# Kernel optimization log

Measured on AMD Instinct MI355X. Metric: run time of the kernel, lower is better.

The kernel has to match this reference:

```python
import jax, jax.numpy as jnp
import numpy as np

N_ATOMS = 50000
N_EDGES = 320000
ATOM_DIM = 32
BOND_DIM = 64


def setup_inputs() -> dict:
    key = jax.random.key(0)
    k1, k2, k3, k4 = jax.random.split(key, 4)
    atom_features = jax.random.normal(k1, (N_ATOMS, ATOM_DIM), dtype=jnp.float32)
    bond_features = jax.random.normal(k2, (N_EDGES, BOND_DIM), dtype=jnp.float32)
    pair_indices = jax.random.randint(k3, (N_EDGES, 2), 0, N_ATOMS, dtype=jnp.int64)
    # Xavier-uniform init for kernel [bond_dim, atom_dim*atom_dim]
    fan_in, fan_out = BOND_DIM, ATOM_DIM * ATOM_DIM
    limit = float(np.sqrt(6.0 / (fan_in + fan_out)))
    kernel = jax.random.uniform(k4, (BOND_DIM, ATOM_DIM * ATOM_DIM), dtype=jnp.float32,
                                minval=-limit, maxval=limit)
    bias = jnp.zeros((ATOM_DIM * ATOM_DIM,), dtype=jnp.float32)
    return {"atom_features": atom_features, "bond_features": bond_features,
            "pair_indices": pair_indices, "kernel": kernel, "bias": bias}


def reference(atom_features, bond_features, pair_indices, kernel, bias):
    d = atom_features.shape[-1]
    # Dense projection: [E, bond_dim] @ [bond_dim, d*d] -> [E, d, d]
    edge_mat = (bond_features @ kernel + bias).reshape(-1, d, d)
    # Gather neighbor features and apply per-edge matrix-vector product
    nbr = atom_features[pair_indices[:, 1]]              # [E, d]
    transformed = jnp.einsum('eij,ej->ei', edge_mat, nbr)  # [E, d]
    # Scatter-add aggregation onto destination atoms
    return jax.ops.segment_sum(transformed, pair_indices[:, 0],
                               num_segments=atom_features.shape[0])
```

## Files before the change

kernel.cpp:

```cpp
#include <hip/hip_runtime.h>
#include <stdint.h>

#define NA 50000
#define NE 320000
#define AD 32
#define BD 64

#define WS_FLAG   0
#define WS_COUNTS 16
#define WS_CURSOR (WS_COUNTS + NA)
#define WS_OFFS   (WS_CURSOR + NA)
#define WS_EIDS   150048

__device__ __forceinline__ void load_pair(const void* p, int e, int mode, int& s, int& d){
  if (mode){ const int* q = (const int*)p; s = q[2*e]; d = q[2*e+1]; }
  else     { const long long* q = (const long long*)p; s = (int)q[2*e]; d = (int)q[2*e+1]; }
}

__global__ void k_detect(const void* pairs, uint32_t* ws){
  const uint32_t* w = (const uint32_t*)pairs;
  uint32_t x = 0;
  for (int i = threadIdx.x; i < 2048; i += 256) x |= w[2*i + 1];
  __shared__ uint32_t sh[256];
  sh[threadIdx.x] = x; __syncthreads();
  for (int s = 128; s > 0; s >>= 1){
    if (threadIdx.x < s) sh[threadIdx.x] |= sh[threadIdx.x + s];
    __syncthreads();
  }
  if (threadIdx.x == 0) ws[WS_FLAG] = (sh[0] != 0u) ? 1u : 0u;
}

__global__ void k_hist(const void* pairs, uint32_t* ws){
  int e = blockIdx.x * 256 + threadIdx.x;
  if (e >= NE) return;
  int mode = (int)ws[WS_FLAG];
  int s, d; load_pair(pairs, e, mode, s, d);
  atomicAdd(&ws[WS_COUNTS + s], 1u);
}

__global__ void k_scan(uint32_t* ws){
  const uint32_t* counts = ws + WS_COUNTS;
  uint32_t* offs = ws + WS_OFFS;
  __shared__ uint32_t wsum[16];
  __shared__ uint32_t carrysh;
  const int tid = threadIdx.x; const int lane = tid & 63; const int wid = tid >> 6;
  if (tid == 0) carrysh = 0u;
  __syncthreads();
  for (int base = 0; base < NA; base += 8192){
    uint32_t v[8]; uint32_t tot = 0u;
    int i0 = base + tid * 8;
    #pragma unroll
    for (int j = 0; j < 8; ++j){ int i = i0 + j; v[j] = (i < NA) ? counts[i] : 0u; tot += v[j]; }
    uint32_t inc = tot;
    #pragma unroll
    for (int m = 1; m < 64; m <<= 1){ uint32_t t = __shfl_up(inc, m); if (lane >= m) inc += t; }
    if (lane == 63) wsum[wid] = inc;
    __syncthreads();
    if (wid == 0){
      uint32_t w = (lane < 16) ? wsum[lane] : 0u;
      #pragma unroll
      for (int m = 1; m < 16; m <<= 1){ uint32_t t = __shfl_up(w, m); if (lane >= m) w += t; }
      if (lane < 16) wsum[lane] = w;
    }
    __syncthreads();
    uint32_t waveoff = (wid == 0) ? 0u : wsum[wid - 1];
    uint32_t run = carrysh + waveoff + (inc - tot);
    #pragma unroll
    for (int j = 0; j < 8; ++j){ int i = i0 + j; if (i < NA) offs[i] = run; run += v[j]; }
    __syncthreads();
    if (tid == 0) carrysh += wsum[15];
    __syncthreads();
  }
  if (tid == 0) offs[NA] = carrysh;
}

__global__ void k_scatter(const void* pairs, uint32_t* ws){
  int e = blockIdx.x * 256 + threadIdx.x;
  if (e >= NE) return;
  int mode = (int)ws[WS_FLAG];
  int s, d; load_pair(pairs, e, mode, s, d);
  uint32_t p = atomicAdd(&ws[WS_CURSOR + s], 1u);
  ws[WS_EIDS + ws[WS_OFFS + s] + p] = (uint32_t)e;
}

__launch_bounds__(512)
__global__ void k_main(const float* __restrict__ atoms, const float* __restrict__ bonds,
                       const void* __restrict__ pairs, const float* __restrict__ Kg,
                       const float* __restrict__ bias, float* __restrict__ out,
                       const uint32_t* __restrict__ ws){
  __shared__ float Ksh[8 * 1024];
  __shared__ float red[8 * 520];

  const int tid  = threadIdx.x;
  const int lane = tid & 63;
  const int wid  = tid >> 6;
  const int kk   = lane & 7;
  const int jq   = lane >> 3;
  const int mode = (int)ws[WS_FLAG];
  const uint32_t* offs = ws + WS_OFFS;
  const uint32_t* eids = ws + WS_EIDS;

  const int a0 = blockIdx.x * 16 + wid * 2;
  const int a1 = a0 + 1;

  float R0[8][4], R1[8][4], S0[4], S1[4];
  #pragma unroll
  for (int c = 0; c < 8; ++c)
    #pragma unroll
    for (int j = 0; j < 4; ++j){ R0[c][j] = 0.f; R1[c][j] = 0.f; }
  #pragma unroll
  for (int j = 0; j < 4; ++j){ S0[j] = 0.f; S1[j] = 0.f; }

  #pragma unroll
  for (int sel = 0; sel < 2; ++sel){
    const int a = sel ? a1 : a0;
    const uint32_t beg = offs[a], end = offs[a + 1];
    for (uint32_t t = beg; t < end; ++t){
      const int e = (int)eids[t];
      int s_, d_; load_pair(pairs, e, mode, s_, d_);
      const float4 av = *(const float4*)&atoms[d_ * AD + jq * 4];
      float b[8];
      #pragma unroll
      for (int c = 0; c < 8; ++c) b[c] = bonds[e * BD + c * 8 + kk];
      if (sel == 0){
        #pragma unroll
        for (int c = 0; c < 8; ++c){
          R0[c][0] += b[c] * av.x; R0[c][1] += b[c] * av.y;
          R0[c][2] += b[c] * av.z; R0[c][3] += b[c] * av.w;
        }
        if (kk == 0){ S0[0] += av.x; S0[1] += av.y; S0[2] += av.z; S0[3] += av.w; }
      } else {
        #pragma unroll
        for (int c = 0; c < 8; ++c){
          R1[c][0] += b[c] * av.x; R1[c][1] += b[c] * av.y;
          R1[c][2] += b[c] * av.z; R1[c][3] += b[c] * av.w;
        }
        if (kk == 0){ S1[0] += av.x; S1[1] += av.y; S1[2] += av.z; S1[3] += av.w; }
      }
    }
  }

  float acc0[32], acc1[32];
  #pragma unroll
  for (int i = 0; i < 32; ++i){ acc0[i] = 0.f; acc1[i] = 0.f; }

  #pragma unroll
  for (int c = 0; c < 8; ++c){
    __syncthreads();
    #pragma unroll
    for (int q = 0; q < 4; ++q){
      int f4 = tid + q * 512;
      int word = f4 * 4;
      int row = word >> 10;
      int col = word & 1023;
      *(float4*)&Ksh[word] = *(const float4*)&Kg[(8 * c + row) * 1024 + col];
    }
    __syncthreads();
    #pragma unroll
    for (int i = 0; i < 32; ++i){
      const float4 kv = *(const float4*)&Ksh[kk * 1024 + i * 32 + jq * 4];
      acc0[i] += kv.x * R0[c][0] + kv.y * R0[c][1] + kv.z * R0[c][2] + kv.w * R0[c][3];
      acc1[i] += kv.x * R1[c][0] + kv.y * R1[c][1] + kv.z * R1[c][2] + kv.w * R1[c][3];
    }
  }

  if (kk == 0){
    #pragma unroll
    for (int i = 0; i < 32; ++i){
      const float4 bv = *(const float4*)&bias[i * 32 + jq * 4];
      acc0[i] += bv.x * S0[0] + bv.y * S0[1] + bv.z * S0[2] + bv.w * S0[3];
      acc1[i] += bv.x * S1[0] + bv.y * S1[1] + bv.z * S1[2] + bv.w * S1[3];
    }
  }

  float* myred = &red[wid * 520];
  auto epi = [&](const float (&acc)[32], int a){
    #pragma unroll
    for (int g = 0; g < 4; ++g){
      #pragma unroll
      for (int ii = 0; ii < 8; ++ii) myred[ii * 65 + lane] = acc[g * 8 + ii];
      const int ii = lane & 7, seg = lane >> 3;
      float p = 0.f;
      #pragma unroll
      for (int t2 = 0; t2 < 8; ++t2) p += myred[ii * 65 + seg * 8 + t2];
      p += __shfl_xor(p, 8);
      p += __shfl_xor(p, 16);
      p += __shfl_xor(p, 32);
      if (lane < 8) out[a * 32 + g * 8 + lane] = p;
    }
  };
  epi(acc0, a0);
  epi(acc1, a1);
}

extern "C" void kernel_launch(void* const* d_in, const int* in_sizes, int n_in,
                              void* d_out, int out_size, void* d_ws, size_t ws_size,
                              hipStream_t stream){
  const float* atoms = (const float*)d_in[0];
  const float* bonds = (const float*)d_in[1];
  const void*  pairs = d_in[2];
  const float* Kg    = (const float*)d_in[3];
  const float* bias  = (const float*)d_in[4];
  float* out = (float*)d_out;
  uint32_t* ws = (uint32_t*)d_ws;

  hipMemsetAsync(ws + WS_COUNTS, 0, sizeof(uint32_t) * 2 * NA, stream);
  k_detect<<<1, 256, 0, stream>>>(pairs, ws);
  k_hist<<<(NE + 255) / 256, 256, 0, stream>>>(pairs, ws);
  k_scan<<<1, 1024, 0, stream>>>(ws);
  k_scatter<<<(NE + 255) / 256, 256, 0, stream>>>(pairs, ws);
  k_main<<<NA / 16, 512, 0, stream>>>(atoms, bonds, pairs, Kg, bias, out, ws);
}
```

Baseline: 1.126 ms.

## Pack edge and neighbor ids, prefetch next edge, vectorize bond loads, swizzle LDS

The scatter pass now stores (edge id, neighbor atom) pairs together when the workspace is large enough. The main kernel then skips the dependent reload of pair_indices. The edge loop software-prefetches the next edge's ids. Bond features are read as two float4 per lane, with the bond-dim mapping changed to kk*8+c and the kernel-row staging reindexed to match. The shared-memory K tile uses an XOR swizzle to reduce bank conflicts, and launch bounds now pin one block per CU. In exchange, the scatter pass writes twice as many bytes, and the code has a second path that depends on workspace size.

```diff
diff --git a/kernel.cpp b/kernel.cpp
--- a/kernel.cpp
+++ b/kernel.cpp
@@ -11,6 +11,8 @@
 #define WS_CURSOR (WS_COUNTS + NA)
 #define WS_OFFS   (WS_CURSOR + NA)
 #define WS_EIDS   150048
+#define WS_NEED_PACKED   ((WS_EIDS + 2 * NE) * 4)
+#define WS_NEED_UNPACKED ((WS_EIDS + NE) * 4)
 
 __device__ __forceinline__ void load_pair(const void* p, int e, int mode, int& s, int& d){
   if (mode){ const int* q = (const int*)p; s = q[2*e]; d = q[2*e+1]; }
@@ -74,20 +76,23 @@
   if (tid == 0) offs[NA] = carrysh;
 }
 
+template<int PACKED>
 __global__ void k_scatter(const void* pairs, uint32_t* ws){
   int e = blockIdx.x * 256 + threadIdx.x;
   if (e >= NE) return;
   int mode = (int)ws[WS_FLAG];
   int s, d; load_pair(pairs, e, mode, s, d);
   uint32_t p = atomicAdd(&ws[WS_CURSOR + s], 1u);
-  ws[WS_EIDS + ws[WS_OFFS + s] + p] = (uint32_t)e;
-}
-
-__launch_bounds__(512)
+  uint32_t pos = ws[WS_OFFS + s] + p;
+  if (PACKED) ((uint2*)(ws + WS_EIDS))[pos] = make_uint2((uint32_t)e, (uint32_t)d);
+  else        ws[WS_EIDS + pos] = (uint32_t)e;
+}
+
+__launch_bounds__(512, 1)
 __global__ void k_main(const float* __restrict__ atoms, const float* __restrict__ bonds,
                        const void* __restrict__ pairs, const float* __restrict__ Kg,
                        const float* __restrict__ bias, float* __restrict__ out,
-                       const uint32_t* __restrict__ ws){
+                       const uint32_t* __restrict__ ws, int packed){
   __shared__ float Ksh[8 * 1024];
   __shared__ float red[8 * 520];
 
@@ -98,7 +103,6 @@
   const int jq   = lane >> 3;
   const int mode = (int)ws[WS_FLAG];
   const uint32_t* offs = ws + WS_OFFS;
-  const uint32_t* eids = ws + WS_EIDS;
 
   const int a0 = blockIdx.x * 16 + wid * 2;
   const int a1 = a0 + 1;
@@ -114,14 +118,29 @@
   #pragma unroll
   for (int sel = 0; sel < 2; ++sel){
     const int a = sel ? a1 : a0;
-    const uint32_t beg = offs[a], end = offs[a + 1];
-    for (uint32_t t = beg; t < end; ++t){
-      const int e = (int)eids[t];
-      int s_, d_; load_pair(pairs, e, mode, s_, d_);
-      const float4 av = *(const float4*)&atoms[d_ * AD + jq * 4];
-      float b[8];
-      #pragma unroll
-      for (int c = 0; c < 8; ++c) b[c] = bonds[e * BD + c * 8 + kk];
+    const uint32_t beg = offs[a];
+    const uint32_t n   = offs[a + 1] - beg;
+    uint32_t e_nxt = 0, d_nxt = 0;
+    if (n){
+      if (packed){ uint2 ed = ((const uint2*)(ws + WS_EIDS))[beg]; e_nxt = ed.x; d_nxt = ed.y; }
+      else {
+        e_nxt = ws[WS_EIDS + beg];
+        int s_, d_; load_pair(pairs, (int)e_nxt, mode, s_, d_); d_nxt = (uint32_t)d_;
+      }
+    }
+    for (uint32_t t = 0; t < n; ++t){
+      const uint32_t e = e_nxt, d = d_nxt;
+      if (t + 1 < n){
+        if (packed){ uint2 ed = ((const uint2*)(ws + WS_EIDS))[beg + t + 1]; e_nxt = ed.x; d_nxt = ed.y; }
+        else {
+          e_nxt = ws[WS_EIDS + beg + t + 1];
+          int s_, d_; load_pair(pairs, (int)e_nxt, mode, s_, d_); d_nxt = (uint32_t)d_;
+        }
+      }
+      const float4 av = *(const float4*)&atoms[d * AD + jq * 4];
+      const float4 b0 = *(const float4*)&bonds[e * BD + kk * 8];
+      const float4 b1 = *(const float4*)&bonds[e * BD + kk * 8 + 4];
+      const float b[8] = {b0.x, b0.y, b0.z, b0.w, b1.x, b1.y, b1.z, b1.w};
       if (sel == 0){
         #pragma unroll
         for (int c = 0; c < 8; ++c){
@@ -149,16 +168,17 @@
     __syncthreads();
     #pragma unroll
     for (int q = 0; q < 4; ++q){
-      int f4 = tid + q * 512;
-      int word = f4 * 4;
-      int row = word >> 10;
-      int col = word & 1023;
-      *(float4*)&Ksh[word] = *(const float4*)&Kg[(8 * c + row) * 1024 + col];
+      const int f4   = tid + q * 512;
+      const int word = f4 * 4;
+      const int row  = word >> 10;
+      const int col  = word & 1023;
+      const int sw   = row * 1024 + (col ^ (row << 2));
+      *(float4*)&Ksh[sw] = *(const float4*)&Kg[(row * 8 + c) * 1024 + col];
     }
     __syncthreads();
     #pragma unroll
     for (int i = 0; i < 32; ++i){
-      const float4 kv = *(const float4*)&Ksh[kk * 1024 + i * 32 + jq * 4];
+      const float4 kv = *(const float4*)&Ksh[kk * 1024 + ((i * 32 + jq * 4) ^ (kk << 2))];
       acc0[i] += kv.x * R0[c][0] + kv.y * R0[c][1] + kv.z * R0[c][2] + kv.w * R0[c][3];
       acc1[i] += kv.x * R1[c][0] + kv.y * R1[c][1] + kv.z * R1[c][2] + kv.w * R1[c][3];
     }
@@ -203,11 +223,13 @@
   const float* bias  = (const float*)d_in[4];
   float* out = (float*)d_out;
   uint32_t* ws = (uint32_t*)d_ws;
+  const int packed = (ws_size >= (size_t)WS_NEED_PACKED) ? 1 : 0;
 
   hipMemsetAsync(ws + WS_COUNTS, 0, sizeof(uint32_t) * 2 * NA, stream);
   k_detect<<<1, 256, 0, stream>>>(pairs, ws);
   k_hist<<<(NE + 255) / 256, 256, 0, stream>>>(pairs, ws);
   k_scan<<<1, 1024, 0, stream>>>(ws);
-  k_scatter<<<(NE + 255) / 256, 256, 0, stream>>>(pairs, ws);
-  k_main<<<NA / 16, 512, 0, stream>>>(atoms, bonds, pairs, Kg, bias, out, ws);
-}
+  if (packed) k_scatter<1><<<(NE + 255) / 256, 256, 0, stream>>>(pairs, ws);
+  else        k_scatter<0><<<(NE + 255) / 256, 256, 0, stream>>>(pairs, ws);
+  k_main<<<NA / 16, 512, 0, stream>>>(atoms, bonds, pairs, Kg, bias, out, ws, packed);
+}
```

After: 1.156 ms. 1.03x slower.

## Pack edge/neighbor ids, vectorize bond loads, read kernel matrix directly from global

Applied to the files above, without the earlier changes.

The scatter pass now stores (edge id, neighbor atom) pairs together when workspace allows, so the main kernel skips the indirect pair lookup. Bond features are loaded as two float4 per lane with a remapped k index, and the contraction reads the weight matrix straight from global/L2 instead of staging it through shared memory with block barriers. Blocks shrink to 256 threads with 8 atoms each, and the contraction is split into two halves to lower register pressure. The trade-off is more global/L2 traffic for the weight matrix and a code path that depends on the workspace size.

```diff
diff --git a/kernel.cpp b/kernel.cpp
--- a/kernel.cpp
+++ b/kernel.cpp
@@ -11,6 +11,7 @@
 #define WS_CURSOR (WS_COUNTS + NA)
 #define WS_OFFS   (WS_CURSOR + NA)
 #define WS_EIDS   150048
+#define WS_NEED_PACKED   ((size_t)(WS_EIDS + 2 * NE) * 4)
 
 __device__ __forceinline__ void load_pair(const void* p, int e, int mode, int& s, int& d){
   if (mode){ const int* q = (const int*)p; s = q[2*e]; d = q[2*e+1]; }
@@ -74,22 +75,81 @@
   if (tid == 0) offs[NA] = carrysh;
 }
 
+template<int PACKED>
 __global__ void k_scatter(const void* pairs, uint32_t* ws){
   int e = blockIdx.x * 256 + threadIdx.x;
   if (e >= NE) return;
   int mode = (int)ws[WS_FLAG];
   int s, d; load_pair(pairs, e, mode, s, d);
   uint32_t p = atomicAdd(&ws[WS_CURSOR + s], 1u);
-  ws[WS_EIDS + ws[WS_OFFS + s] + p] = (uint32_t)e;
-}
-
-__launch_bounds__(512)
+  uint32_t pos = ws[WS_OFFS + s] + p;
+  if (PACKED) ((uint2*)(ws + WS_EIDS))[pos] = make_uint2((uint32_t)e, (uint32_t)d);
+  else        ws[WS_EIDS + pos] = (uint32_t)e;
+}
+
+#define F4Z make_float4(0.f, 0.f, 0.f, 0.f)
+#define FMA4(dst, v, s) { dst.x += (v).x*(s); dst.y += (v).y*(s); dst.z += (v).z*(s); dst.w += (v).w*(s); }
+#define ADD4(dst, v)    { dst.x += (v).x; dst.y += (v).y; dst.z += (v).z; dst.w += (v).w; }
+
+#define EDGE_LOOP(A, Q0,Q1,Q2,Q3,Q4,Q5,Q6,Q7, SS)                                   \
+  { const uint32_t beg = offs[A], endv = offs[(A)+1];                               \
+    for (uint32_t t = beg; t < endv; ++t){                                          \
+      uint32_t e_, d_;                                                              \
+      if (PACKED){ const uint2 ed = eds[t]; e_ = ed.x; d_ = ed.y; }                 \
+      else { e_ = eids[t]; int ss_, dd_; load_pair(pairs, (int)e_, mode, ss_, dd_); d_ = (uint32_t)dd_; } \
+      const float4 av  = *(const float4*)&atoms[d_ * AD + jq * 4];                  \
+      const float4 b0v = *(const float4*)&bonds[e_ * BD + kk * 8];                  \
+      const float4 b1v = *(const float4*)&bonds[e_ * BD + kk * 8 + 4];              \
+      FMA4(Q0, av, b0v.x) FMA4(Q1, av, b0v.y) FMA4(Q2, av, b0v.z) FMA4(Q3, av, b0v.w) \
+      FMA4(Q4, av, b1v.x) FMA4(Q5, av, b1v.y) FMA4(Q6, av, b1v.z) FMA4(Q7, av, b1v.w) \
+      if (kk == 0) ADD4(SS, av)                                                     \
+    } }
+
+#define COMP0 x
+#define COMP1 y
+#define COMP2 z
+#define COMP3 w
+#define CDOT(acc, comp, kv, r) acc.comp += (kv).x*(r).x + (kv).y*(r).y + (kv).z*(r).z + (kv).w*(r).w;
+
+#define CSTEP(c, h, g, io)                                                          \
+  { const float4 kv = *(const float4*)&Kg[(kk*8+(c))*1024 + (h)*512 + ((g)*4+(io))*32 + jq*4]; \
+    CDOT(aA##g, COMP##io, kv, r0_##c) CDOT(aB##g, COMP##io, kv, r1_##c) }
+#define CSTEP4(c, h, g)  CSTEP(c,h,g,0) CSTEP(c,h,g,1) CSTEP(c,h,g,2) CSTEP(c,h,g,3)
+#define CBLOCK(c, h)     CSTEP4(c,h,0) CSTEP4(c,h,1) CSTEP4(c,h,2) CSTEP4(c,h,3)
+#define CONTRACT_ALLC(h) CBLOCK(0,h) CBLOCK(1,h) CBLOCK(2,h) CBLOCK(3,h) \
+                         CBLOCK(4,h) CBLOCK(5,h) CBLOCK(6,h) CBLOCK(7,h)
+
+#define BSTEP(h, g, io)                                                             \
+  { const float4 bv = *(const float4*)&bias[((h)*16+(g)*4+(io))*32 + jq*4];         \
+    CDOT(aA##g, COMP##io, bv, S0) CDOT(aB##g, COMP##io, bv, S1) }
+#define BSTEP4(h, g) BSTEP(h,g,0) BSTEP(h,g,1) BSTEP(h,g,2) BSTEP(h,g,3)
+#define BIAS_ALL(h)  BSTEP4(h,0) BSTEP4(h,1) BSTEP4(h,2) BSTEP4(h,3)
+
+#define EPI8(v0, v1, g, h, a)                                                       \
+  { myred[0*65+lane]=v0.x; myred[1*65+lane]=v0.y; myred[2*65+lane]=v0.z; myred[3*65+lane]=v0.w; \
+    myred[4*65+lane]=v1.x; myred[5*65+lane]=v1.y; myred[6*65+lane]=v1.z; myred[7*65+lane]=v1.w; \
+    const int ii2 = lane & 7, seg = lane >> 3;                                      \
+    float p = myred[ii2*65+seg*8+0] + myred[ii2*65+seg*8+1] + myred[ii2*65+seg*8+2] \
+            + myred[ii2*65+seg*8+3] + myred[ii2*65+seg*8+4] + myred[ii2*65+seg*8+5] \
+            + myred[ii2*65+seg*8+6] + myred[ii2*65+seg*8+7];                        \
+    p += __shfl_xor(p, 8); p += __shfl_xor(p, 16); p += __shfl_xor(p, 32);          \
+    if (lane < 8) out[(a)*32 + (h)*16 + (g)*8 + lane] = p; }
+
+#define CONTRACT_HALF(h)                                                            \
+  { float4 aA0=F4Z, aA1=F4Z, aA2=F4Z, aA3=F4Z;                                      \
+    float4 aB0=F4Z, aB1=F4Z, aB2=F4Z, aB3=F4Z;                                      \
+    CONTRACT_ALLC(h)                                                                \
+    if (kk == 0){ BIAS_ALL(h) }                                                     \
+    EPI8(aA0, aA1, 0, h, a0) EPI8(aA2, aA3, 1, h, a0)                               \
+    EPI8(aB0, aB1, 0, h, a1) EPI8(aB2, aB3, 1, h, a1) }
+
+template<int PACKED>
+__launch_bounds__(256, 1)
 __global__ void k_main(const float* __restrict__ atoms, const float* __restrict__ bonds,
                        const void* __restrict__ pairs, const float* __restrict__ Kg,
                        const float* __restrict__ bias, float* __restrict__ out,
                        const uint32_t* __restrict__ ws){
-  __shared__ float Ksh[8 * 1024];
-  __shared__ float red[8 * 520];
+  __shared__ float red[4 * 520];
 
   const int tid  = threadIdx.x;
   const int lane = tid & 63;
@@ -99,98 +159,22 @@
   const int mode = (int)ws[WS_FLAG];
   const uint32_t* offs = ws + WS_OFFS;
   const uint32_t* eids = ws + WS_EIDS;
-
-  const int a0 = blockIdx.x * 16 + wid * 2;
+  const uint2*    eds  = (const uint2*)(ws + WS_EIDS);
+  (void)mode; (void)eids; (void)eds;
+
+  const int a0 = blockIdx.x * 8 + wid * 2;
   const int a1 = a0 + 1;
 
-  float R0[8][4], R1[8][4], S0[4], S1[4];
-  #pragma unroll
-  for (int c = 0; c < 8; ++c)
-    #pragma unroll
-    for (int j = 0; j < 4; ++j){ R0[c][j] = 0.f; R1[c][j] = 0.f; }
-  #pragma unroll
-  for (int j = 0; j < 4; ++j){ S0[j] = 0.f; S1[j] = 0.f; }
-
-  #pragma unroll
-  for (int sel = 0; sel < 2; ++sel){
-    const int a = sel ? a1 : a0;
-    const uint32_t beg = offs[a], end = offs[a + 1];
-    for (uint32_t t = beg; t < end; ++t){
-      const int e = (int)eids[t];
-      int s_, d_; load_pair(pairs, e, mode, s_, d_);
-      const float4 av = *(const float4*)&atoms[d_ * AD + jq * 4];
-      float b[8];
-      #pragma unroll
-      for (int c = 0; c < 8; ++c) b[c] = bonds[e * BD + c * 8 + kk];
-      if (sel == 0){
-        #pragma unroll
-        for (int c = 0; c < 8; ++c){
-          R0[c][0] += b[c] * av.x; R0[c][1] += b[c] * av.y;
-          R0[c][2] += b[c] * av.z; R0[c][3] += b[c] * av.w;
-        }
-        if (kk == 0){ S0[0] += av.x; S0[1] += av.y; S0[2] += av.z; S0[3] += av.w; }
-      } else {
-        #pragma unroll
-        for (int c = 0; c < 8; ++c){
-          R1[c][0] += b[c] * av.x; R1[c][1] += b[c] * av.y;
-          R1[c][2] += b[c] * av.z; R1[c][3] += b[c] * av.w;
-        }
-        if (kk == 0){ S1[0] += av.x; S1[1] += av.y; S1[2] += av.z; S1[3] += av.w; }
-      }
-    }
-  }
-
-  float acc0[32], acc1[32];
-  #pragma unroll
-  for (int i = 0; i < 32; ++i){ acc0[i] = 0.f; acc1[i] = 0.f; }
-
-  #pragma unroll
-  for (int c = 0; c < 8; ++c){
-    __syncthreads();
-    #pragma unroll
-    for (int q = 0; q < 4; ++q){
-      int f4 = tid + q * 512;
-      int word = f4 * 4;
-      int row = word >> 10;
-      int col = word & 1023;
-      *(float4*)&Ksh[word] = *(const float4*)&Kg[(8 * c + row) * 1024 + col];
-    }
-    __syncthreads();
-    #pragma unroll
-    for (int i = 0; i < 32; ++i){
-      const float4 kv = *(const float4*)&Ksh[kk * 1024 + i * 32 + jq * 4];
-      acc0[i] += kv.x * R0[c][0] + kv.y * R0[c][1] + kv.z * R0[c][2] + kv.w * R0[c][3];
-      acc1[i] += kv.x * R1[c][0] + kv.y * R1[c][1] + kv.z * R1[c][2] + kv.w * R1[c][3];
-    }
-  }
-
-  if (kk == 0){
-    #pragma unroll
-    for (int i = 0; i < 32; ++i){
-      const float4 bv = *(const float4*)&bias[i * 32 + jq * 4];
-      acc0[i] += bv.x * S0[0] + bv.y * S0[1] + bv.z * S0[2] + bv.w * S0[3];
-      acc1[i] += bv.x * S1[0] + bv.y * S1[1] + bv.z * S1[2] + bv.w * S1[3];
-    }
-  }
+  float4 r0_0=F4Z, r0_1=F4Z, r0_2=F4Z, r0_3=F4Z, r0_4=F4Z, r0_5=F4Z, r0_6=F4Z, r0_7=F4Z;
+  float4 r1_0=F4Z, r1_1=F4Z, r1_2=F4Z, r1_3=F4Z, r1_4=F4Z, r1_5=F4Z, r1_6=F4Z, r1_7=F4Z;
+  float4 S0=F4Z, S1=F4Z;
+
+  EDGE_LOOP(a0, r0_0,r0_1,r0_2,r0_3,r0_4,r0_5,r0_6,r0_7, S0)
+  EDGE_LOOP(a1, r1_0,r1_1,r1_2,r1_3,r1_4,r1_5,r1_6,r1_7, S1)
 
   float* myred = &red[wid * 520];
-  auto epi = [&](const float (&acc)[32], int a){
-    #pragma unroll
-    for (int g = 0; g < 4; ++g){
-      #pragma unroll
-      for (int ii = 0; ii < 8; ++ii) myred[ii * 65 + lane] = acc[g * 8 + ii];
-      const int ii = lane & 7, seg = lane >> 3;
-      float p = 0.f;
-      #pragma unroll
-      for (int t2 = 0; t2 < 8; ++t2) p += myred[ii * 65 + seg * 8 + t2];
-      p += __shfl_xor(p, 8);
-      p += __shfl_xor(p, 16);
-      p += __shfl_xor(p, 32);
-      if (lane < 8) out[a * 32 + g * 8 + lane] = p;
-    }
-  };
-  epi(acc0, a0);
-  epi(acc1, a1);
+  CONTRACT_HALF(0)
+  CONTRACT_HALF(1)
 }
 
 extern "C" void kernel_launch(void* const* d_in, const int* in_sizes, int n_in,
@@ -203,11 +187,17 @@
   const float* bias  = (const float*)d_in[4];
   float* out = (float*)d_out;
   uint32_t* ws = (uint32_t*)d_ws;
+  const int packed = (ws_size >= WS_NEED_PACKED) ? 1 : 0;
 
   hipMemsetAsync(ws + WS_COUNTS, 0, sizeof(uint32_t) * 2 * NA, stream);
   k_detect<<<1, 256, 0, stream>>>(pairs, ws);
   k_hist<<<(NE + 255) / 256, 256, 0, stream>>>(pairs, ws);
   k_scan<<<1, 1024, 0, stream>>>(ws);
-  k_scatter<<<(NE + 255) / 256, 256, 0, stream>>>(pairs, ws);
-  k_main<<<NA / 16, 512, 0, stream>>>(atoms, bonds, pairs, Kg, bias, out, ws);
-}
+  if (packed){
+    k_scatter<1><<<(NE + 255) / 256, 256, 0, stream>>>(pairs, ws);
+    k_main<1><<<NA / 8, 256, 0, stream>>>(atoms, bonds, pairs, Kg, bias, out, ws);
+  } else {
+    k_scatter<0><<<(NE + 255) / 256, 256, 0, stream>>>(pairs, ws);
+    k_main<0><<<NA / 8, 256, 0, stream>>>(atoms, bonds, pairs, Kg, bias, out, ws);
+  }
+}
```

Measured after the change: 1.236 ms. 9.8% more time.
